# Performance work log

Hardware: AMD Instinct MI355X
Metric: run time of the kernel (lower is better)

## Reference

```python
import jax, jax.numpy as jnp
import numpy as np
from jax import lax

B_, L_, D_ = 4, 2048, 256
DI, NS, DC, DTR = 512, 16, 4, 16  # d_inner=2*D, d_state, d_conv, dt_rank=ceil(D/16)
DFF = 4 * D_


def setup_inputs():
    key = jax.random.key(0)
    ks = jax.random.split(key, 20)
    rn = lambda k, s, sc=0.02: jax.random.normal(k, s, jnp.float32) * sc
    return {
        "x": jax.random.normal(ks[0], (B_, L_, D_), jnp.float32),
        "in_proj_w": rn(ks[1], (2 * DI, D_)), "in_proj_b": jnp.zeros((2 * DI,), jnp.float32),
        "conv_w": rn(ks[2], (DI, DC), 0.1), "conv_b": jnp.zeros((DI,), jnp.float32),
        "x_proj_w": rn(ks[3], (DTR + 2 * NS, DI)),
        "dt_proj_w": rn(ks[4], (DI, DTR), 0.1), "dt_proj_b": rn(ks[5], (DI,), 0.5),
        "A_log": jnp.log(jnp.tile(jnp.arange(1, NS + 1, dtype=jnp.float32), (DI, 1))),
        "D_ssm": jnp.ones((DI,), jnp.float32),
        "out_proj_w": rn(ks[6], (D_, DI)), "out_proj_b": jnp.zeros((D_,), jnp.float32),
        "ln1_g": jnp.ones((D_,), jnp.float32), "ln1_b": jnp.zeros((D_,), jnp.float32),
        "fc1_w": rn(ks[7], (DFF, D_)), "fc1_b": jnp.zeros((DFF,), jnp.float32),
        "fc2_w": rn(ks[8], (D_, DFF)), "fc2_b": jnp.zeros((D_,), jnp.float32),
        "ln2_g": jnp.ones((D_,), jnp.float32), "ln2_b": jnp.zeros((D_,), jnp.float32),
    }


def _layer_norm(x, g, b, eps=1e-5):
    m = jnp.mean(x, -1, keepdims=True)
    v = jnp.mean((x - m) ** 2, -1, keepdims=True)
    return (x - m) / jnp.sqrt(v + eps) * g + b


def _mamba(x, in_proj_w, in_proj_b, conv_w, conv_b, x_proj_w, dt_proj_w, dt_proj_b, A_log, D_ssm, out_proj_w, out_proj_b):
    B, L, D = x.shape
    xz = x @ in_proj_w.T + in_proj_b                       # [B,L,2*DI]
    xi, z = jnp.split(xz, 2, axis=-1)
    # causal depthwise conv over time
    xc = jnp.transpose(xi, (0, 2, 1))                       # [B,DI,L]
    xc = lax.conv_general_dilated(xc, conv_w[:, None, :], (1,), [(DC - 1, 0)],
                                  dimension_numbers=("NCH", "OIH", "NCH"),
                                  feature_group_count=DI)
    xi = jax.nn.silu(jnp.transpose(xc + conv_b[None, :, None], (0, 2, 1)))  # [B,L,DI]
    x_dbl = xi @ x_proj_w.T                                 # [B,L,DTR+2*NS]
    dt, Bs, Cs = jnp.split(x_dbl, [DTR, DTR + NS], axis=-1)
    dt = jax.nn.softplus(dt @ dt_proj_w.T + dt_proj_b)      # [B,L,DI]
    A = -jnp.exp(A_log)                                     # [DI,NS]
    dA = jnp.exp(dt[..., None] * A)                         # [B,L,DI,NS]
    dBu = dt[..., None] * Bs[:, :, None, :] * xi[..., None]  # [B,L,DI,NS]
    dA_t = jnp.moveaxis(dA, 1, 0)
    dBu_t = jnp.moveaxis(dBu, 1, 0)
    C_t = jnp.moveaxis(Cs, 1, 0)                            # [L,B,NS]

    def step(h, inp):
        a, bu, c = inp
        h = a * h + bu                                      # [B,DI,NS]
        y = jnp.einsum("bdn,bn->bd", h, c)
        return h, y

    h0 = jnp.zeros((B, DI, NS), x.dtype)
    _, ys = lax.scan(step, h0, (dA_t, dBu_t, C_t))
    y = jnp.moveaxis(ys, 0, 1) + xi * D_ssm                 # [B,L,DI]
    y = y * jax.nn.silu(z)
    return y @ out_proj_w.T + out_proj_b


def reference(x, in_proj_w, in_proj_b, conv_w, conv_b, x_proj_w, dt_proj_w, dt_proj_b,
              A_log, D_ssm, out_proj_w, out_proj_b, ln1_g, ln1_b, fc1_w, fc1_b,
              fc2_w, fc2_b, ln2_g, ln2_b):
    gelu = lambda t: jax.nn.gelu(t, approximate=False)
    ssm = _mamba(x, in_proj_w, in_proj_b, conv_w, conv_b, x_proj_w, dt_proj_w,
                 dt_proj_b, A_log, D_ssm, out_proj_w, out_proj_b)
    y = _layer_norm(x + ssm, ln1_g, ln1_b)                  # dropout = identity (eval)
    ffn = gelu(gelu(y @ fc1_w.T + fc1_b) @ fc2_w.T + fc2_b)
    return _layer_norm(y + ffn, ln2_g, ln2_b)
```

## Files before the change

kernel.cpp:

```cpp
#include <hip/hip_runtime.h>

typedef __bf16 bf16x8 __attribute__((ext_vector_type(8)));
typedef float  f32x4  __attribute__((ext_vector_type(4)));

#define AS1 __attribute__((address_space(1)))
#define AS3 __attribute__((address_space(3)))

__device__ __forceinline__ float bf2f(ushort u) {
    union { unsigned int i; float f; } v; v.i = ((unsigned int)u) << 16; return v.f;
}
__device__ __forceinline__ ushort f2bf(float f) {
    union { float f; unsigned int i; } v; v.f = f;
    unsigned int i = v.i;
    unsigned int r = i + 0x7FFFu + ((i >> 16) & 1u);
    return (ushort)(r >> 16);
}
__device__ __forceinline__ float bflo(unsigned int u) { return bf2f((ushort)(u & 0xFFFFu)); }
__device__ __forceinline__ float bfhi(unsigned int u) { return bf2f((ushort)(u >> 16)); }
__device__ __forceinline__ float gelu_f(float v) {
    return 0.5f * v * (1.f + erff(v * 0.70710678118654752f));
}

__device__ __forceinline__ bool sniff_inline(const ushort* __restrict__ x) {
    const int lane = threadIdx.x & 63;
    int cnt = 0;
    #pragma unroll
    for (int r = 0; r < 4; r++) {
        const ushort u = x[lane + r * 64];
        const int e = (u >> 7) & 0xFF;
        if ((u & 0x7FFF) == 0 || (e >= 112 && e <= 141)) cnt++;
    }
    #pragma unroll
    for (int o = 32; o > 0; o >>= 1) cnt += __shfl_xor(cnt, o);
    return cnt >= 224;
}

struct CanonArgs {
    const void* src[20];
    int off[20];
    int total;
};

__launch_bounds__(256)
__global__ void canon_k(CanonArgs a, ushort* __restrict__ dst, ushort* __restrict__ xpw_pad,
                        const ushort* __restrict__ sniffx)
{
    const int i = blockIdx.x * 256 + threadIdx.x;
    if (i >= a.total) {
        const int j = i - a.total;
        if (j < 8192) xpw_pad[24576 + j] = 0;
        return;
    }
    const bool fl = sniff_inline(sniffx);
    int s = 0;
    #pragma unroll
    for (int t = 1; t < 20; t++) if (i >= a.off[t]) s = t;
    const int li = i - a.off[s];
    ushort v;
    if (fl) v = ((const ushort*)a.src[s])[li];
    else    v = f2bf(((const float*)a.src[s])[li]);
    dst[i] = v;
    if (s == 5) xpw_pad[li] = v;
}

template<int BM, int BN>
__launch_bounds__(256, 2)
__global__ void gemm_bt(const ushort* __restrict__ A, const ushort* __restrict__ W,
                        const ushort* __restrict__ bias, ushort* __restrict__ Cb,
                        int N, int K)
{
    constexpr int WMT = BM / 32;
    constexpr int WNT = BN / 32;
    __shared__ __align__(16) ushort As[BM * 32];
    __shared__ __align__(16) ushort Bs[BN * 32];
    const int tid  = threadIdx.x;
    const int wave = tid >> 6;
    const int lane = tid & 63;
    const int m0 = blockIdx.x * BM;
    const int n0 = blockIdx.y * BN;
    const int wm = (wave >> 1) * (BM / 2);
    const int wn = (wave & 1) * (BN / 2);
    const int lrow = lane & 15;
    const int quad = lane >> 4;

    f32x4 acc[WMT][WNT];
    #pragma unroll
    for (int i = 0; i < WMT; i++)
        #pragma unroll
        for (int j = 0; j < WNT; j++)
            #pragma unroll
            for (int r = 0; r < 4; r++) acc[i][j][r] = 0.f;

    for (int k0 = 0; k0 < K; k0 += 32) {
        #pragma unroll
        for (int t = 0; t < BM / 64; t++) {
            const int inst = t * 4 + wave;
            const int row  = inst * 16 + (lane >> 2);
            const int sub  = lane & 3;
            const ushort* gp = A + (size_t)(m0 + row) * K + (k0 + sub * 8);
            __builtin_amdgcn_global_load_lds((AS1 void*)(void*)gp,
                                             (AS3 void*)(As + inst * 512), 16, 0, 0);
        }
        #pragma unroll
        for (int t = 0; t < BN / 64; t++) {
            const int inst = t * 4 + wave;
            const int row  = inst * 16 + (lane >> 2);
            const int sub  = lane & 3;
            const ushort* gp = W + (size_t)(n0 + row) * K + (k0 + sub * 8);
            __builtin_amdgcn_global_load_lds((AS1 void*)(void*)gp,
                                             (AS3 void*)(Bs + inst * 512), 16, 0, 0);
        }
        __syncthreads();
        bf16x8 afr[WMT], bfr[WNT];
        #pragma unroll
        for (int i = 0; i < WMT; i++)
            afr[i] = *(const bf16x8*)&As[(wm + i * 16 + lrow) * 32 + quad * 8];
        #pragma unroll
        for (int j = 0; j < WNT; j++)
            bfr[j] = *(const bf16x8*)&Bs[(wn + j * 16 + lrow) * 32 + quad * 8];
        #pragma unroll
        for (int i = 0; i < WMT; i++)
            #pragma unroll
            for (int j = 0; j < WNT; j++)
                acc[i][j] = __builtin_amdgcn_mfma_f32_16x16x32_bf16(afr[i], bfr[j], acc[i][j], 0, 0, 0);
        __syncthreads();
    }

    #pragma unroll
    for (int i = 0; i < WMT; i++) {
        const int gm = m0 + wm + i * 16 + quad * 4;
        #pragma unroll
        for (int j = 0; j < WNT; j++) {
            const int gn = n0 + wn + j * 16 + lrow;
            const float bv = bf2f(bias[gn]);
            #pragma unroll
            for (int r = 0; r < 4; r++)
                Cb[(size_t)(gm + r) * N + gn] = f2bf(acc[i][j][r] + bv);
        }
    }
}

__launch_bounds__(512)
__global__ void convscan1_k(const ushort* __restrict__ xz, const ushort* __restrict__ cw,
                            const ushort* __restrict__ cb, const ushort* __restrict__ xpw_pad,
                            const ushort* __restrict__ dtw, const ushort* __restrict__ dtb,
                            const ushort* __restrict__ Alog,
                            float* __restrict__ xdbl, float* __restrict__ summh,
                            float* __restrict__ sdt32, float* __restrict__ hhalf,
                            float* __restrict__ sdthalf)
{
    __shared__ __align__(16) ushort xcs[32 * 520];
    __shared__ float XD[32 * 48];
    const int tid  = threadIdx.x;
    const int wave = tid >> 6;
    const int lane = tid & 63;
    const int lrow = lane & 15;
    const int quad = lane >> 4;
    const int c = blockIdx.x, b = blockIdx.y;
    const int t0 = b * 2048 + c * 32;

    {
        const int d8 = (tid & 63) * 8;
        ushort wl[32];
        *(uint4*)&wl[0]  = *(const uint4*)&cw[d8 * 4];
        *(uint4*)&wl[8]  = *(const uint4*)&cw[d8 * 4 + 8];
        *(uint4*)&wl[16] = *(const uint4*)&cw[d8 * 4 + 16];
        *(uint4*)&wl[24] = *(const uint4*)&cw[d8 * 4 + 24];
        ushort bl[8];
        *(uint4*)&bl[0] = *(const uint4*)&cb[d8];
        #pragma unroll
        for (int it = 0; it < 4; it++) {
            const int trow = it * 8 + wave;
            const int t = t0 + trow;
            const int l = t & 2047;
            float acc[8];
            #pragma unroll
            for (int j = 0; j < 8; j++) acc[j] = bf2f(bl[j]);
            #pragma unroll
            for (int k = 0; k < 4; k++) {
                const int ls = l - 3 + k;
                if (ls >= 0) {
                    ushort xl[8];
                    *(uint4*)&xl[0] = *(const uint4*)&xz[(size_t)(t - 3 + k) * 1024 + d8];
                    #pragma unroll
                    for (int j = 0; j < 8; j++) acc[j] += bf2f(xl[j]) * bf2f(wl[j * 4 + k]);
                }
            }
            ushort ol[8];
            #pragma unroll
            for (int j = 0; j < 8; j++) {
                const float s = acc[j] / (1.f + __expf(-acc[j]));
                ol[j] = f2bf(s);
            }
            *(uint4*)&xcs[trow * 520 + d8] = *(uint4*)&ol[0];
        }
    }
    __syncthreads();

    {
        const int mt = wave >> 2, nt = wave & 3;
        const ushort* bptr = xpw_pad + (size_t)(nt * 16 + lrow) * 512 + quad * 8;
        f32x4 acc = {0.f, 0.f, 0.f, 0.f};
        #pragma unroll
        for (int hh = 0; hh < 2; hh++) {
            bf16x8 Bv[8];
            #pragma unroll
            for (int s = 0; s < 8; s++)
                Bv[s] = *(const bf16x8*)(bptr + hh * 256 + s * 32);
            #pragma unroll
            for (int s = 0; s < 8; s++) {
                const bf16x8 afr = *(const bf16x8*)&xcs[(mt * 16 + lrow) * 520 + hh * 256 + s * 32 + quad * 8];
                acc = __builtin_amdgcn_mfma_f32_16x16x32_bf16(afr, Bv[s], acc, 0, 0, 0);
            }
        }
        const int col = nt * 16 + lrow;
        if (col < 48) {
            #pragma unroll
            for (int r = 0; r < 4; r++) {
                const int row = mt * 16 + quad * 4 + r;
                XD[row * 48 + col] = acc[r];
                xdbl[(size_t)(t0 + row) * 64 + col] = acc[r];
            }
        }
    }
    __syncthreads();

    {
        const int d = tid;
        const uint4 w0 = *(const uint4*)&dtw[d * 16];
        const uint4 w1 = *(const uint4*)&dtw[d * 16 + 8];
        const float wd[16] = { bflo(w0.x), bfhi(w0.x), bflo(w0.y), bfhi(w0.y),
                               bflo(w0.z), bfhi(w0.z), bflo(w0.w), bfhi(w0.w),
                               bflo(w1.x), bfhi(w1.x), bflo(w1.y), bfhi(w1.y),
                               bflo(w1.z), bfhi(w1.z), bflo(w1.w), bfhi(w1.w) };
        const float dtbv = bf2f(dtb[d]);
        float A[16], h[16];
        #pragma unroll
        for (int n = 0; n < 16; n++) {
            A[n] = -__expf(bf2f(Alog[d * 16 + n]));
            h[n] = 0.f;
        }
        const size_t bh = ((size_t)(b * 64 + c) * 16) * 512 + d;
        const size_t bs = (size_t)(b * 64 + c) * 512 + d;
        float sdt = 0.f;
        for (int i = 0; i < 32; i++) {
            const float* Xr = &XD[i * 48];
            float s0 = dtbv, s1 = 0.f, s2 = 0.f, s3 = 0.f;
            #pragma unroll
            for (int k = 0; k < 16; k += 4) {
                s0 += Xr[k]     * wd[k];
                s1 += Xr[k + 1] * wd[k + 1];
                s2 += Xr[k + 2] * wd[k + 2];
                s3 += Xr[k + 3] * wd[k + 3];
            }
            const float s = (s0 + s1) + (s2 + s3);
            const float dtv = (s > 15.f) ? s : __logf(1.f + __expf(s));
            const float xiv = bf2f(xcs[i * 520 + d]);
            const float dx = dtv * xiv;
            sdt += dtv;
            #pragma unroll
            for (int n = 0; n < 16; n++) {
                const float da = __expf(dtv * A[n]);
                h[n] = da * h[n] + dx * Xr[16 + n];
            }
            if (i == 15) {
                #pragma unroll
                for (int n = 0; n < 16; n++) hhalf[bh + (size_t)n * 512] = h[n];
                sdthalf[bs] = sdt;
            }
        }
        #pragma unroll
        for (int n = 0; n < 16; n++) summh[bh + (size_t)n * 512] = h[n];
        sdt32[bs] = sdt;
    }
}

__launch_bounds__(128)
__global__ void combine_k(float* __restrict__ summh, const float* __restrict__ sdt32,
                          const ushort* __restrict__ Alog)
{
    const int b  = blockIdx.x >> 6;
    const int n  = (blockIdx.x >> 2) & 15;
    const int dq = blockIdx.x & 3;
    const int d  = dq * 128 + threadIdx.x;
    const float An = -__expf(bf2f(Alog[d * 16 + n]));
    float h = 0.f;
    #pragma unroll
    for (int q = 0; q < 2; q++) {
        float p[32], hl[32], ho[32];
        #pragma unroll
        for (int c2 = 0; c2 < 32; c2++) {
            const int cc = q * 32 + c2;
            hl[c2] = summh[((size_t)(b * 64 + cc) * 16 + n) * 512 + d];
            p[c2]  = __expf(An * sdt32[(size_t)(b * 64 + cc) * 512 + d]);
        }
        #pragma unroll
        for (int c2 = 0; c2 < 32; c2++) {
            ho[c2] = h;
            h = p[c2] * h + hl[c2];
        }
        #pragma unroll
        for (int c2 = 0; c2 < 32; c2++)
            summh[((size_t)(b * 64 + (q * 32 + c2)) * 16 + n) * 512 + d] = ho[c2];
    }
}

__launch_bounds__(512, 4)
__global__ void tail_k(const ushort* __restrict__ xz, const ushort* __restrict__ cw,
                       const ushort* __restrict__ cb, const float* __restrict__ xdbl,
                       const ushort* __restrict__ dtw, const ushort* __restrict__ dtb,
                       const ushort* __restrict__ Alog, const float* __restrict__ summh,
                       const float* __restrict__ hhalf, const float* __restrict__ sdthalf,
                       const ushort* __restrict__ Dssm, const ushort* __restrict__ cx,
                       const ushort* __restrict__ opw, const ushort* __restrict__ opb,
                       const ushort* __restrict__ ln1g, const ushort* __restrict__ ln1b,
                       const ushort* __restrict__ f1w, const ushort* __restrict__ f1b,
                       const ushort* __restrict__ f2w, const ushort* __restrict__ f2b,
                       const ushort* __restrict__ ln2g, const ushort* __restrict__ ln2b,
                       void* __restrict__ dout, const ushort* __restrict__ sniffx)
{
    __shared__ __align__(16) ushort yls[16 * 520];
    __shared__ float XD[16 * 48];
    __shared__ __align__(16) ushort y1bs[16 * 264];
    __shared__ float redS[8 * 16], redQ[8 * 16];
    ushort* f1q = yls;

    const int tid  = threadIdx.x;
    const int wave = tid >> 6;
    const int lane = tid & 63;
    const int lrow = lane & 15;
    const int quad = lane >> 4;
    const int c = blockIdx.x, b = blockIdx.y;
    const int t0 = b * 2048 + c * 16;
    const int n0w = wave * 32;

    {
        const int d8 = (tid & 63) * 8;
        ushort wl[32];
        *(uint4*)&wl[0]  = *(const uint4*)&cw[d8 * 4];
        *(uint4*)&wl[8]  = *(const uint4*)&cw[d8 * 4 + 8];
        *(uint4*)&wl[16] = *(const uint4*)&cw[d8 * 4 + 16];
        *(uint4*)&wl[24] = *(const uint4*)&cw[d8 * 4 + 24];
        ushort bl[8];
        *(uint4*)&bl[0] = *(const uint4*)&cb[d8];
        #pragma unroll
        for (int it = 0; it < 2; it++) {
            const int trow = it * 8 + wave;
            const int t = t0 + trow;
            const int l = t & 2047;
            float acc[8];
            #pragma unroll
            for (int j = 0; j < 8; j++) acc[j] = bf2f(bl[j]);
            #pragma unroll
            for (int k = 0; k < 4; k++) {
                const int ls = l - 3 + k;
                if (ls >= 0) {
                    ushort xl[8];
                    *(uint4*)&xl[0] = *(const uint4*)&xz[(size_t)(t - 3 + k) * 1024 + d8];
                    #pragma unroll
                    for (int j = 0; j < 8; j++) acc[j] += bf2f(xl[j]) * bf2f(wl[j * 4 + k]);
                }
            }
            ushort ol[8];
            #pragma unroll
            for (int j = 0; j < 8; j++) {
                const float s = acc[j] / (1.f + __expf(-acc[j]));
                ol[j] = f2bf(s);
            }
            *(uint4*)&yls[trow * 520 + d8] = *(uint4*)&ol[0];
        }
    }
    for (int e = tid; e < 768; e += 512)
        XD[e] = xdbl[(size_t)(t0 + (e / 48)) * 64 + (e % 48)];
    __syncthreads();

    {
        const int d = tid;
        const uint4 w0 = *(const uint4*)&dtw[d * 16];
        const uint4 w1 = *(const uint4*)&dtw[d * 16 + 8];
        const float wd[16] = { bflo(w0.x), bfhi(w0.x), bflo(w0.y), bfhi(w0.y),
                               bflo(w0.z), bfhi(w0.z), bflo(w0.w), bfhi(w0.w),
                               bflo(w1.x), bfhi(w1.x), bflo(w1.y), bfhi(w1.y),
                               bflo(w1.z), bfhi(w1.z), bflo(w1.w), bfhi(w1.w) };
        const float dtbv = bf2f(dtb[d]);
        float A[16], h[16];
        #pragma unroll
        for (int n = 0; n < 16; n++) A[n] = -__expf(bf2f(Alog[d * 16 + n]));
        const int c32 = c >> 1;
        const size_t bh = ((size_t)(b * 64 + c32) * 16) * 512 + d;
        #pragma unroll
        for (int n = 0; n < 16; n++) h[n] = summh[bh + (size_t)n * 512];
        if (c & 1) {
            const float sdth = sdthalf[(size_t)(b * 64 + c32) * 512 + d];
            #pragma unroll
            for (int n = 0; n < 16; n++)
                h[n] = __expf(A[n] * sdth) * h[n] + hhalf[bh + (size_t)n * 512];
        }
        const float Dv = bf2f(Dssm[d]);
        for (int i = 0; i < 16; i++) {
            const int t = t0 + i;
            const float* Xr = &XD[i * 48];
            float s0 = dtbv, s1 = 0.f, s2 = 0.f, s3 = 0.f;
            #pragma unroll
            for (int k = 0; k < 16; k += 4) {
                s0 += Xr[k]     * wd[k];
                s1 += Xr[k + 1] * wd[k + 1];
                s2 += Xr[k + 2] * wd[k + 2];
                s3 += Xr[k + 3] * wd[k + 3];
            }
            const float s = (s0 + s1) + (s2 + s3);
            const float dtv = (s > 15.f) ? s : __logf(1.f + __expf(s));
            const float xiv = bf2f(yls[i * 520 + d]);
            const float dx = dtv * xiv;
            float yv0 = 0.f, yv1 = 0.f;
            #pragma unroll
            for (int n = 0; n < 16; n += 2) {
                const float da0 = __expf(dtv * A[n]);
                const float da1 = __expf(dtv * A[n + 1]);
                h[n]     = da0 * h[n]     + dx * Xr[16 + n];
                h[n + 1] = da1 * h[n + 1] + dx * Xr[17 + n];
                yv0 += h[n]     * Xr[32 + n];
                yv1 += h[n + 1] * Xr[33 + n];
            }
            float yv = yv0 + yv1;
            yv += xiv * Dv;
            const float zv = bf2f(xz[(size_t)t * 1024 + 512 + d]);
            yv *= zv / (1.f + __expf(-zv));
            yls[i * 520 + d] = f2bf(yv);
        }
    }
    __syncthreads();

    f32x4 accP[2];
    #pragma unroll
    for (int j = 0; j < 2; j++)
        #pragma unroll
        for (int r = 0; r < 4; r++) accP[j][r] = 0.f;
    {
        const ushort* bp0 = opw + (size_t)(n0w + lrow) * 512 + quad * 8;
        const ushort* bp1 = opw + (size_t)(n0w + 16 + lrow) * 512 + quad * 8;
        #pragma unroll
        for (int hh = 0; hh < 2; hh++) {
            bf16x8 B0[8], B1[8];
            #pragma unroll
            for (int s = 0; s < 8; s++) {
                B0[s] = *(const bf16x8*)(bp0 + hh * 256 + s * 32);
                B1[s] = *(const bf16x8*)(bp1 + hh * 256 + s * 32);
            }
            #pragma unroll
            for (int s = 0; s < 8; s++) {
                const bf16x8 afr = *(const bf16x8*)&yls[lrow * 520 + hh * 256 + s * 32 + quad * 8];
                accP[0] = __builtin_amdgcn_mfma_f32_16x16x32_bf16(afr, B0[s], accP[0], 0, 0, 0);
                accP[1] = __builtin_amdgcn_mfma_f32_16x16x32_bf16(afr, B1[s], accP[1], 0, 0, 0);
            }
        }
    }
    float vP[2][4];
    float ps[4], pq[4];
    #pragma unroll
    for (int r = 0; r < 4; r++) { ps[r] = 0.f; pq[r] = 0.f; }
    #pragma unroll
    for (int j = 0; j < 2; j++) {
        const int col = n0w + j * 16 + lrow;
        const float bv = bf2f(opb[col]);
        #pragma unroll
        for (int r = 0; r < 4; r++) {
            const int row = quad * 4 + r;
            float v = accP[j][r] + bv + bf2f(cx[(size_t)(t0 + row) * 256 + col]);
            vP[j][r] = v;
            ps[r] += v;
            pq[r] += v * v;
        }
    }
    #pragma unroll
    for (int r = 0; r < 4; r++) {
        #pragma unroll
        for (int o = 8; o > 0; o >>= 1) {
            ps[r] += __shfl_xor(ps[r], o);
            pq[r] += __shfl_xor(pq[r], o);
        }
        if (lrow == 0) {
            const int row = quad * 4 + r;
            redS[wave * 16 + row] = ps[r];
            redQ[wave * 16 + row] = pq[r];
        }
    }
    __syncthreads();

    float y1f[2][4];
    #pragma unroll
    for (int r = 0; r < 4; r++) {
        const int row = quad * 4 + r;
        float S = 0.f, Q = 0.f;
        #pragma unroll
        for (int w = 0; w < 8; w++) { S += redS[w * 16 + row]; Q += redQ[w * 16 + row]; }
        const float mean = S * (1.f / 256.f);
        const float var  = Q * (1.f / 256.f) - mean * mean;
        const float rs   = rsqrtf(var + 1e-5f);
        #pragma unroll
        for (int j = 0; j < 2; j++) {
            const int col = n0w + j * 16 + lrow;
            const float o2 = (vP[j][r] - mean) * rs * bf2f(ln1g[col]) + bf2f(ln1b[col]);
            y1f[j][r] = o2;
            y1bs[row * 264 + col] = f2bf(o2);
        }
    }
    __syncthreads();

    f32x4 acc2[2];
    #pragma unroll
    for (int j = 0; j < 2; j++)
        #pragma unroll
        for (int r = 0; r < 4; r++) acc2[j][r] = 0.f;

    for (int q = 0; q < 4; q++) {
        f32x4 a1[2];
        #pragma unroll
        for (int j = 0; j < 2; j++)
            #pragma unroll
            for (int r = 0; r < 4; r++) a1[j][r] = 0.f;
        {
            const ushort* bp0 = f1w + (size_t)(q * 256 + n0w + lrow) * 256 + quad * 8;
            const ushort* bp1 = f1w + (size_t)(q * 256 + n0w + 16 + lrow) * 256 + quad * 8;
            bf16x8 B0[8], B1[8];
            #pragma unroll
            for (int s = 0; s < 8; s++) {
                B0[s] = *(const bf16x8*)(bp0 + s * 32);
                B1[s] = *(const bf16x8*)(bp1 + s * 32);
            }
            #pragma unroll
            for (int s = 0; s < 8; s++) {
                const bf16x8 afr = *(const bf16x8*)&y1bs[lrow * 264 + s * 32 + quad * 8];
                a1[0] = __builtin_amdgcn_mfma_f32_16x16x32_bf16(afr, B0[s], a1[0], 0, 0, 0);
                a1[1] = __builtin_amdgcn_mfma_f32_16x16x32_bf16(afr, B1[s], a1[1], 0, 0, 0);
            }
        }
        #pragma unroll
        for (int j = 0; j < 2; j++) {
            const int qc = n0w + j * 16 + lrow;
            const float bv = bf2f(f1b[q * 256 + qc]);
            #pragma unroll
            for (int r = 0; r < 4; r++) {
                const int row = quad * 4 + r;
                f1q[row * 260 + qc] = f2bf(gelu_f(a1[j][r] + bv));
            }
        }
        __syncthreads();
        {
            const ushort* bp0 = f2w + (size_t)(n0w + lrow) * 1024 + q * 256 + quad * 8;
            const ushort* bp1 = f2w + (size_t)(n0w + 16 + lrow) * 1024 + q * 256 + quad * 8;
            bf16x8 B0[8], B1[8];
            #pragma unroll
            for (int s = 0; s < 8; s++) {
                B0[s] = *(const bf16x8*)(bp0 + s * 32);
                B1[s] = *(const bf16x8*)(bp1 + s * 32);
            }
            #pragma unroll
            for (int s = 0; s < 8; s++) {
                const bf16x8 afr = *(const bf16x8*)&f1q[lrow * 260 + s * 32 + quad * 8];
                acc2[0] = __builtin_amdgcn_mfma_f32_16x16x32_bf16(afr, B0[s], acc2[0], 0, 0, 0);
                acc2[1] = __builtin_amdgcn_mfma_f32_16x16x32_bf16(afr, B1[s], acc2[1], 0, 0, 0);
            }
        }
        __syncthreads();
    }

    float v2[2][4];
    #pragma unroll
    for (int r = 0; r < 4; r++) { ps[r] = 0.f; pq[r] = 0.f; }
    #pragma unroll
    for (int j = 0; j < 2; j++) {
        const int col = n0w + j * 16 + lrow;
        const float bv = bf2f(f2b[col]);
        #pragma unroll
        for (int r = 0; r < 4; r++) {
            const float v = gelu_f(acc2[j][r] + bv) + y1f[j][r];
            v2[j][r] = v;
            ps[r] += v;
            pq[r] += v * v;
        }
    }
    #pragma unroll
    for (int r = 0; r < 4; r++) {
        #pragma unroll
        for (int o = 8; o > 0; o >>= 1) {
            ps[r] += __shfl_xor(ps[r], o);
            pq[r] += __shfl_xor(pq[r], o);
        }
        if (lrow == 0) {
            const int row = quad * 4 + r;
            redS[wave * 16 + row] = ps[r];
            redQ[wave * 16 + row] = pq[r];
        }
    }
    __syncthreads();

    const bool fl = sniff_inline(sniffx);
    #pragma unroll
    for (int r = 0; r < 4; r++) {
        const int row = quad * 4 + r;
        float S = 0.f, Q = 0.f;
        #pragma unroll
        for (int w = 0; w < 8; w++) { S += redS[w * 16 + row]; Q += redQ[w * 16 + row]; }
        const float mean = S * (1.f / 256.f);
        const float var  = Q * (1.f / 256.f) - mean * mean;
        const float rs   = rsqrtf(var + 1e-5f);
        #pragma unroll
        for (int j = 0; j < 2; j++) {
            const int col = n0w + j * 16 + lrow;
            const size_t off = (size_t)(t0 + row) * 256 + col;
            const float o2 = (v2[j][r] - mean) * rs * bf2f(ln2g[col]) + bf2f(ln2b[col]);
            if (fl) ((ushort*)dout)[off] = f2bf(o2);
            else    ((float*)dout)[off]  = o2;
        }
    }
}

extern "C" void kernel_launch(void* const* d_in, const int* in_sizes, int n_in,
                              void* d_out, int out_size, void* d_ws, size_t ws_size,
                              hipStream_t stream)
{
    char* ws = (char*)d_ws;
    ushort* canon = (ushort*)(ws + 256);

    static const int coff[20] = {
        0,        2097152,  2359296,  2360320,  2362368,
        2362880,  2387456,  2395648,  2396160,  2404352,
        2404864,  2535936,  2536192,  2536448,  2536704,
        2798848,  2799872,  3062016,  3062272,  3062528 };
    static const int ctot = 3062784;

    CanonArgs ca;
    for (int i = 0; i < 20; i++) { ca.src[i] = d_in[i]; ca.off[i] = coff[i]; }
    ca.total = ctot;

    const ushort* cx   = canon + coff[0];
    const ushort* cipw = canon + coff[1];
    const ushort* cipb = canon + coff[2];
    const ushort* ccw  = canon + coff[3];
    const ushort* ccb  = canon + coff[4];
    const ushort* cdtw = canon + coff[6];
    const ushort* cdtb = canon + coff[7];
    const ushort* calog= canon + coff[8];
    const ushort* cdssm= canon + coff[9];
    const ushort* copw = canon + coff[10];
    const ushort* copb = canon + coff[11];
    const ushort* cln1g= canon + coff[12];
    const ushort* cln1b= canon + coff[13];
    const ushort* cf1w = canon + coff[14];
    const ushort* cf1b = canon + coff[15];
    const ushort* cf2w = canon + coff[16];
    const ushort* cf2b = canon + coff[17];
    const ushort* cln2g= canon + coff[18];
    const ushort* cln2b= canon + coff[19];

    ushort* xpw_pad = (ushort*)(ws + 6291456);
    ushort* xz      = (ushort*)(ws + 8388608);
    float*  xdbl    = (float*)(ws + 25165824);
    float*  summh   = (float*)(ws + 27262976);
    float*  hhalf   = (float*)(ws + 35651584);
    float*  sdt32   = (float*)(ws + 44040192);
    float*  sdthalf = (float*)(ws + 44564480);
    const ushort* sx = (const ushort*)d_in[0];

    canon_k<<<(ctot + 8192 + 255) / 256, 256, 0, stream>>>(ca, canon, xpw_pad, sx);
    gemm_bt<128, 128><<<dim3(64, 8), 256, 0, stream>>>(cx, cipw, cipb, xz, 1024, 256);
    convscan1_k<<<dim3(64, 4), 512, 0, stream>>>(
        xz, ccw, ccb, xpw_pad, cdtw, cdtb, calog, xdbl, summh, sdt32, hhalf, sdthalf);
    combine_k<<<256, 128, 0, stream>>>(summh, sdt32, calog);
    tail_k<<<dim3(128, 4), 512, 0, stream>>>(
        xz, ccw, ccb, xdbl, cdtw, cdtb, calog, summh, hhalf, sdthalf, cdssm, cx,
        copw, copb, cln1g, cln1b, cf1w, cf1b, cf2w, cf2b, cln2g, cln2b,
        d_out, sx);
}
```

Baseline: 255.5 us.

## Split conv/scan pipeline into separate kernels with finer 16-step chunks

Replaces the fused conv+scan1 kernel and the tail kernel's scan prologue with separate conv/x_proj, scan1, combine and scan2 kernels. Chunks shrink from 32 to 16 timesteps and the channel dimension is split across blocks, so the serial scans run on more, smaller blocks (1024 instead of 256). The conv output is materialised to global memory and scan2 writes gated y back into xz, which the FFN kernel then reads. This adds two kernel launches and extra global traffic but removes the duplicated conv work and the half-chunk fixup in the tail kernel, and shortens the per-block serial dependency chain.

```diff
diff --git a/kernel.cpp b/kernel.cpp
--- a/kernel.cpp
+++ b/kernel.cpp
@@ -141,23 +141,18 @@
 }
 
 __launch_bounds__(512)
-__global__ void convscan1_k(const ushort* __restrict__ xz, const ushort* __restrict__ cw,
-                            const ushort* __restrict__ cb, const ushort* __restrict__ xpw_pad,
-                            const ushort* __restrict__ dtw, const ushort* __restrict__ dtb,
-                            const ushort* __restrict__ Alog,
-                            float* __restrict__ xdbl, float* __restrict__ summh,
-                            float* __restrict__ sdt32, float* __restrict__ hhalf,
-                            float* __restrict__ sdthalf)
-{
-    __shared__ __align__(16) ushort xcs[32 * 520];
-    __shared__ float XD[32 * 48];
+__global__ void convx_k(const ushort* __restrict__ xz, const ushort* __restrict__ cw,
+                        const ushort* __restrict__ cb, const ushort* __restrict__ xpw_pad,
+                        ushort* __restrict__ xc, float* __restrict__ xdbl)
+{
+    __shared__ __align__(16) ushort xcs[16 * 520];
     const int tid  = threadIdx.x;
     const int wave = tid >> 6;
     const int lane = tid & 63;
     const int lrow = lane & 15;
     const int quad = lane >> 4;
     const int c = blockIdx.x, b = blockIdx.y;
-    const int t0 = b * 2048 + c * 32;
+    const int t0 = b * 2048 + c * 16;
 
     {
         const int d8 = (tid & 63) * 8;
@@ -169,7 +164,7 @@
         ushort bl[8];
         *(uint4*)&bl[0] = *(const uint4*)&cb[d8];
         #pragma unroll
-        for (int it = 0; it < 4; it++) {
+        for (int it = 0; it < 2; it++) {
             const int trow = it * 8 + wave;
             const int t = t0 + trow;
             const int l = t & 2047;
@@ -197,8 +192,8 @@
     }
     __syncthreads();
 
-    {
-        const int mt = wave >> 2, nt = wave & 3;
+    if (wave < 3) {
+        const int nt = wave;
         const ushort* bptr = xpw_pad + (size_t)(nt * 16 + lrow) * 512 + quad * 8;
         f32x4 acc = {0.f, 0.f, 0.f, 0.f};
         #pragma unroll
@@ -209,74 +204,88 @@
                 Bv[s] = *(const bf16x8*)(bptr + hh * 256 + s * 32);
             #pragma unroll
             for (int s = 0; s < 8; s++) {
-                const bf16x8 afr = *(const bf16x8*)&xcs[(mt * 16 + lrow) * 520 + hh * 256 + s * 32 + quad * 8];
+                const bf16x8 afr = *(const bf16x8*)&xcs[lrow * 520 + hh * 256 + s * 32 + quad * 8];
                 acc = __builtin_amdgcn_mfma_f32_16x16x32_bf16(afr, Bv[s], acc, 0, 0, 0);
             }
         }
         const int col = nt * 16 + lrow;
         if (col < 48) {
             #pragma unroll
-            for (int r = 0; r < 4; r++) {
-                const int row = mt * 16 + quad * 4 + r;
-                XD[row * 48 + col] = acc[r];
-                xdbl[(size_t)(t0 + row) * 64 + col] = acc[r];
-            }
-        }
-    }
+            for (int r = 0; r < 4; r++)
+                xdbl[(size_t)(t0 + quad * 4 + r) * 64 + col] = acc[r];
+        }
+    }
+
+    {
+        const int row = tid >> 5;
+        const int col = (tid & 31) * 16;
+        *(uint4*)&xc[(size_t)(t0 + row) * 512 + col]     = *(const uint4*)&xcs[row * 520 + col];
+        *(uint4*)&xc[(size_t)(t0 + row) * 512 + col + 8] = *(const uint4*)&xcs[row * 520 + col + 8];
+    }
+}
+
+__launch_bounds__(256)
+__global__ void scan1_k(const ushort* __restrict__ xc, const float* __restrict__ xdbl,
+                        const ushort* __restrict__ dtw, const ushort* __restrict__ dtb,
+                        const ushort* __restrict__ Alog,
+                        float* __restrict__ summh, float* __restrict__ sdtb)
+{
+    __shared__ float XD[16 * 48];
+    const int tid = threadIdx.x;
+    const int c = blockIdx.x, dh = blockIdx.y, b = blockIdx.z;
+    const int t0 = b * 2048 + c * 16;
+    const int d = dh * 256 + tid;
+
+    for (int e = tid; e < 768; e += 256)
+        XD[e] = xdbl[(size_t)(t0 + (e / 48)) * 64 + (e % 48)];
     __syncthreads();
 
-    {
-        const int d = tid;
-        const uint4 w0 = *(const uint4*)&dtw[d * 16];
-        const uint4 w1 = *(const uint4*)&dtw[d * 16 + 8];
-        const float wd[16] = { bflo(w0.x), bfhi(w0.x), bflo(w0.y), bfhi(w0.y),
-                               bflo(w0.z), bfhi(w0.z), bflo(w0.w), bfhi(w0.w),
-                               bflo(w1.x), bfhi(w1.x), bflo(w1.y), bfhi(w1.y),
-                               bflo(w1.z), bfhi(w1.z), bflo(w1.w), bfhi(w1.w) };
-        const float dtbv = bf2f(dtb[d]);
-        float A[16], h[16];
+    const uint4 w0 = *(const uint4*)&dtw[d * 16];
+    const uint4 w1 = *(const uint4*)&dtw[d * 16 + 8];
+    const float wd[16] = { bflo(w0.x), bfhi(w0.x), bflo(w0.y), bfhi(w0.y),
+                           bflo(w0.z), bfhi(w0.z), bflo(w0.w), bfhi(w0.w),
+                           bflo(w1.x), bfhi(w1.x), bflo(w1.y), bfhi(w1.y),
+                           bflo(w1.z), bfhi(w1.z), bflo(w1.w), bfhi(w1.w) };
+    const uint4 a0 = *(const uint4*)&Alog[d * 16];
+    const uint4 a1 = *(const uint4*)&Alog[d * 16 + 8];
+    const float al[16] = { bflo(a0.x), bfhi(a0.x), bflo(a0.y), bfhi(a0.y),
+                           bflo(a0.z), bfhi(a0.z), bflo(a0.w), bfhi(a0.w),
+                           bflo(a1.x), bfhi(a1.x), bflo(a1.y), bfhi(a1.y),
+                           bflo(a1.z), bfhi(a1.z), bflo(a1.w), bfhi(a1.w) };
+    const float dtbv = bf2f(dtb[d]);
+    float A[16], h[16];
+    #pragma unroll
+    for (int n = 0; n < 16; n++) { A[n] = -__expf(al[n]); h[n] = 0.f; }
+    float sdt = 0.f;
+    for (int i = 0; i < 16; i++) {
+        const float* Xr = &XD[i * 48];
+        float s0 = dtbv, s1 = 0.f, s2 = 0.f, s3 = 0.f;
+        #pragma unroll
+        for (int k = 0; k < 16; k += 4) {
+            s0 += Xr[k]     * wd[k];
+            s1 += Xr[k + 1] * wd[k + 1];
+            s2 += Xr[k + 2] * wd[k + 2];
+            s3 += Xr[k + 3] * wd[k + 3];
+        }
+        const float s = (s0 + s1) + (s2 + s3);
+        const float dtv = (s > 15.f) ? s : __logf(1.f + __expf(s));
+        const float xiv = bf2f(xc[(size_t)(t0 + i) * 512 + d]);
+        const float dx = dtv * xiv;
+        sdt += dtv;
         #pragma unroll
         for (int n = 0; n < 16; n++) {
-            A[n] = -__expf(bf2f(Alog[d * 16 + n]));
-            h[n] = 0.f;
-        }
-        const size_t bh = ((size_t)(b * 64 + c) * 16) * 512 + d;
-        const size_t bs = (size_t)(b * 64 + c) * 512 + d;
-        float sdt = 0.f;
-        for (int i = 0; i < 32; i++) {
-            const float* Xr = &XD[i * 48];
-            float s0 = dtbv, s1 = 0.f, s2 = 0.f, s3 = 0.f;
-            #pragma unroll
-            for (int k = 0; k < 16; k += 4) {
-                s0 += Xr[k]     * wd[k];
-                s1 += Xr[k + 1] * wd[k + 1];
-                s2 += Xr[k + 2] * wd[k + 2];
-                s3 += Xr[k + 3] * wd[k + 3];
-            }
-            const float s = (s0 + s1) + (s2 + s3);
-            const float dtv = (s > 15.f) ? s : __logf(1.f + __expf(s));
-            const float xiv = bf2f(xcs[i * 520 + d]);
-            const float dx = dtv * xiv;
-            sdt += dtv;
-            #pragma unroll
-            for (int n = 0; n < 16; n++) {
-                const float da = __expf(dtv * A[n]);
-                h[n] = da * h[n] + dx * Xr[16 + n];
-            }
-            if (i == 15) {
-                #pragma unroll
-                for (int n = 0; n < 16; n++) hhalf[bh + (size_t)n * 512] = h[n];
-                sdthalf[bs] = sdt;
-            }
-        }
-        #pragma unroll
-        for (int n = 0; n < 16; n++) summh[bh + (size_t)n * 512] = h[n];
-        sdt32[bs] = sdt;
-    }
+            const float da = __expf(dtv * A[n]);
+            h[n] = da * h[n] + dx * Xr[16 + n];
+        }
+    }
+    const size_t bh = ((size_t)(b * 128 + c) * 16) * 512 + d;
+    #pragma unroll
+    for (int n = 0; n < 16; n++) summh[bh + (size_t)n * 512] = h[n];
+    sdtb[(size_t)(b * 128 + c) * 512 + d] = sdt;
 }
 
 __launch_bounds__(128)
-__global__ void combine_k(float* __restrict__ summh, const float* __restrict__ sdt32,
+__global__ void combine_k(float* __restrict__ summh, const float* __restrict__ sdtb,
                           const ushort* __restrict__ Alog)
 {
     const int b  = blockIdx.x >> 6;
@@ -286,13 +295,13 @@
     const float An = -__expf(bf2f(Alog[d * 16 + n]));
     float h = 0.f;
     #pragma unroll
-    for (int q = 0; q < 2; q++) {
+    for (int q = 0; q < 4; q++) {
         float p[32], hl[32], ho[32];
         #pragma unroll
         for (int c2 = 0; c2 < 32; c2++) {
             const int cc = q * 32 + c2;
-            hl[c2] = summh[((size_t)(b * 64 + cc) * 16 + n) * 512 + d];
-            p[c2]  = __expf(An * sdt32[(size_t)(b * 64 + cc) * 512 + d]);
+            hl[c2] = summh[((size_t)(b * 128 + cc) * 16 + n) * 512 + d];
+            p[c2]  = __expf(An * sdtb[(size_t)(b * 128 + cc) * 512 + d]);
         }
         #pragma unroll
         for (int c2 = 0; c2 < 32; c2++) {
@@ -301,26 +310,91 @@
         }
         #pragma unroll
         for (int c2 = 0; c2 < 32; c2++)
-            summh[((size_t)(b * 64 + (q * 32 + c2)) * 16 + n) * 512 + d] = ho[c2];
+            summh[((size_t)(b * 128 + (q * 32 + c2)) * 16 + n) * 512 + d] = ho[c2];
+    }
+}
+
+__launch_bounds__(256)
+__global__ void scan2_k(ushort* __restrict__ xz, const ushort* __restrict__ xc,
+                        const float* __restrict__ xdbl,
+                        const ushort* __restrict__ dtw, const ushort* __restrict__ dtb,
+                        const ushort* __restrict__ Alog, const float* __restrict__ summh,
+                        const ushort* __restrict__ Dssm)
+{
+    __shared__ float XD[16 * 48];
+    const int tid = threadIdx.x;
+    const int c = blockIdx.x, dh = blockIdx.y, b = blockIdx.z;
+    const int t0 = b * 2048 + c * 16;
+    const int d = dh * 256 + tid;
+
+    for (int e = tid; e < 768; e += 256)
+        XD[e] = xdbl[(size_t)(t0 + (e / 48)) * 64 + (e % 48)];
+    __syncthreads();
+
+    const uint4 w0 = *(const uint4*)&dtw[d * 16];
+    const uint4 w1 = *(const uint4*)&dtw[d * 16 + 8];
+    const float wd[16] = { bflo(w0.x), bfhi(w0.x), bflo(w0.y), bfhi(w0.y),
+                           bflo(w0.z), bfhi(w0.z), bflo(w0.w), bfhi(w0.w),
+                           bflo(w1.x), bfhi(w1.x), bflo(w1.y), bfhi(w1.y),
+                           bflo(w1.z), bfhi(w1.z), bflo(w1.w), bfhi(w1.w) };
+    const uint4 a0 = *(const uint4*)&Alog[d * 16];
+    const uint4 a1 = *(const uint4*)&Alog[d * 16 + 8];
+    const float al[16] = { bflo(a0.x), bfhi(a0.x), bflo(a0.y), bfhi(a0.y),
+                           bflo(a0.z), bfhi(a0.z), bflo(a0.w), bfhi(a0.w),
+                           bflo(a1.x), bfhi(a1.x), bflo(a1.y), bfhi(a1.y),
+                           bflo(a1.z), bfhi(a1.z), bflo(a1.w), bfhi(a1.w) };
+    const float dtbv = bf2f(dtb[d]);
+    float A[16], h[16];
+    #pragma unroll
+    for (int n = 0; n < 16; n++) A[n] = -__expf(al[n]);
+    const size_t bh = ((size_t)(b * 128 + c) * 16) * 512 + d;
+    #pragma unroll
+    for (int n = 0; n < 16; n++) h[n] = summh[bh + (size_t)n * 512];
+    const float Dv = bf2f(Dssm[d]);
+
+    for (int i = 0; i < 16; i++) {
+        const int t = t0 + i;
+        const float* Xr = &XD[i * 48];
+        float s0 = dtbv, s1 = 0.f, s2 = 0.f, s3 = 0.f;
+        #pragma unroll
+        for (int k = 0; k < 16; k += 4) {
+            s0 += Xr[k]     * wd[k];
+            s1 += Xr[k + 1] * wd[k + 1];
+            s2 += Xr[k + 2] * wd[k + 2];
+            s3 += Xr[k + 3] * wd[k + 3];
+        }
+        const float s = (s0 + s1) + (s2 + s3);
+        const float dtv = (s > 15.f) ? s : __logf(1.f + __expf(s));
+        const float xiv = bf2f(xc[(size_t)t * 512 + d]);
+        const float dx = dtv * xiv;
+        float yv0 = 0.f, yv1 = 0.f;
+        #pragma unroll
+        for (int n = 0; n < 16; n += 2) {
+            const float da0 = __expf(dtv * A[n]);
+            const float da1 = __expf(dtv * A[n + 1]);
+            h[n]     = da0 * h[n]     + dx * Xr[16 + n];
+            h[n + 1] = da1 * h[n + 1] + dx * Xr[17 + n];
+            yv0 += h[n]     * Xr[32 + n];
+            yv1 += h[n + 1] * Xr[33 + n];
+        }
+        float yv = yv0 + yv1;
+        yv += xiv * Dv;
+        const float zv = bf2f(xz[(size_t)t * 1024 + 512 + d]);
+        yv *= zv / (1.f + __expf(-zv));
+        xz[(size_t)t * 1024 + d] = f2bf(yv);
     }
 }
 
 __launch_bounds__(512, 4)
-__global__ void tail_k(const ushort* __restrict__ xz, const ushort* __restrict__ cw,
-                       const ushort* __restrict__ cb, const float* __restrict__ xdbl,
-                       const ushort* __restrict__ dtw, const ushort* __restrict__ dtb,
-                       const ushort* __restrict__ Alog, const float* __restrict__ summh,
-                       const float* __restrict__ hhalf, const float* __restrict__ sdthalf,
-                       const ushort* __restrict__ Dssm, const ushort* __restrict__ cx,
-                       const ushort* __restrict__ opw, const ushort* __restrict__ opb,
-                       const ushort* __restrict__ ln1g, const ushort* __restrict__ ln1b,
-                       const ushort* __restrict__ f1w, const ushort* __restrict__ f1b,
-                       const ushort* __restrict__ f2w, const ushort* __restrict__ f2b,
-                       const ushort* __restrict__ ln2g, const ushort* __restrict__ ln2b,
-                       void* __restrict__ dout, const ushort* __restrict__ sniffx)
+__global__ void ffn_k(const ushort* __restrict__ xz, const ushort* __restrict__ cx,
+                      const ushort* __restrict__ opw, const ushort* __restrict__ opb,
+                      const ushort* __restrict__ ln1g, const ushort* __restrict__ ln1b,
+                      const ushort* __restrict__ f1w, const ushort* __restrict__ f1b,
+                      const ushort* __restrict__ f2w, const ushort* __restrict__ f2b,
+                      const ushort* __restrict__ ln2g, const ushort* __restrict__ ln2b,
+                      void* __restrict__ dout, const ushort* __restrict__ sniffx)
 {
     __shared__ __align__(16) ushort yls[16 * 520];
-    __shared__ float XD[16 * 48];
     __shared__ __align__(16) ushort y1bs[16 * 264];
     __shared__ float redS[8 * 16], redQ[8 * 16];
     ushort* f1q = yls;
@@ -335,99 +409,10 @@
     const int n0w = wave * 32;
 
     {
-        const int d8 = (tid & 63) * 8;
-        ushort wl[32];
-        *(uint4*)&wl[0]  = *(const uint4*)&cw[d8 * 4];
-        *(uint4*)&wl[8]  = *(const uint4*)&cw[d8 * 4 + 8];
-        *(uint4*)&wl[16] = *(const uint4*)&cw[d8 * 4 + 16];
-        *(uint4*)&wl[24] = *(const uint4*)&cw[d8 * 4 + 24];
-        ushort bl[8];
-        *(uint4*)&bl[0] = *(const uint4*)&cb[d8];
-        #pragma unroll
-        for (int it = 0; it < 2; it++) {
-            const int trow = it * 8 + wave;
-            const int t = t0 + trow;
-            const int l = t & 2047;
-            float acc[8];
-            #pragma unroll
-            for (int j = 0; j < 8; j++) acc[j] = bf2f(bl[j]);
-            #pragma unroll
-            for (int k = 0; k < 4; k++) {
-                const int ls = l - 3 + k;
-                if (ls >= 0) {
-                    ushort xl[8];
-                    *(uint4*)&xl[0] = *(const uint4*)&xz[(size_t)(t - 3 + k) * 1024 + d8];
-                    #pragma unroll
-                    for (int j = 0; j < 8; j++) acc[j] += bf2f(xl[j]) * bf2f(wl[j * 4 + k]);
-                }
-            }
-            ushort ol[8];
-            #pragma unroll
-            for (int j = 0; j < 8; j++) {
-                const float s = acc[j] / (1.f + __expf(-acc[j]));
-                ol[j] = f2bf(s);
-            }
-            *(uint4*)&yls[trow * 520 + d8] = *(uint4*)&ol[0];
-        }
-    }
-    for (int e = tid; e < 768; e += 512)
-        XD[e] = xdbl[(size_t)(t0 + (e / 48)) * 64 + (e % 48)];
-    __syncthreads();
-
-    {
-        const int d = tid;
-        const uint4 w0 = *(const uint4*)&dtw[d * 16];
-        const uint4 w1 = *(const uint4*)&dtw[d * 16 + 8];
-        const float wd[16] = { bflo(w0.x), bfhi(w0.x), bflo(w0.y), bfhi(w0.y),
-                               bflo(w0.z), bfhi(w0.z), bflo(w0.w), bfhi(w0.w),
-                               bflo(w1.x), bfhi(w1.x), bflo(w1.y), bfhi(w1.y),
-                               bflo(w1.z), bfhi(w1.z), bflo(w1.w), bfhi(w1.w) };
-        const float dtbv = bf2f(dtb[d]);
-        float A[16], h[16];
-        #pragma unroll
-        for (int n = 0; n < 16; n++) A[n] = -__expf(bf2f(Alog[d * 16 + n]));
-        const int c32 = c >> 1;
-        const size_t bh = ((size_t)(b * 64 + c32) * 16) * 512 + d;
-        #pragma unroll
-        for (int n = 0; n < 16; n++) h[n] = summh[bh + (size_t)n * 512];
-        if (c & 1) {
-            const float sdth = sdthalf[(size_t)(b * 64 + c32) * 512 + d];
-            #pragma unroll
-            for (int n = 0; n < 16; n++)
-                h[n] = __expf(A[n] * sdth) * h[n] + hhalf[bh + (size_t)n * 512];
-        }
-        const float Dv = bf2f(Dssm[d]);
-        for (int i = 0; i < 16; i++) {
-            const int t = t0 + i;
-            const float* Xr = &XD[i * 48];
-            float s0 = dtbv, s1 = 0.f, s2 = 0.f, s3 = 0.f;
-            #pragma unroll
-            for (int k = 0; k < 16; k += 4) {
-                s0 += Xr[k]     * wd[k];
-                s1 += Xr[k + 1] * wd[k + 1];
-                s2 += Xr[k + 2] * wd[k + 2];
-                s3 += Xr[k + 3] * wd[k + 3];
-            }
-            const float s = (s0 + s1) + (s2 + s3);
-            const float dtv = (s > 15.f) ? s : __logf(1.f + __expf(s));
-            const float xiv = bf2f(yls[i * 520 + d]);
-            const float dx = dtv * xiv;
-            float yv0 = 0.f, yv1 = 0.f;
-            #pragma unroll
-            for (int n = 0; n < 16; n += 2) {
-                const float da0 = __expf(dtv * A[n]);
-                const float da1 = __expf(dtv * A[n + 1]);
-                h[n]     = da0 * h[n]     + dx * Xr[16 + n];
-                h[n + 1] = da1 * h[n + 1] + dx * Xr[17 + n];
-                yv0 += h[n]     * Xr[32 + n];
-                yv1 += h[n + 1] * Xr[33 + n];
-            }
-            float yv = yv0 + yv1;
-            yv += xiv * Dv;
-            const float zv = bf2f(xz[(size_t)t * 1024 + 512 + d]);
-            yv *= zv / (1.f + __expf(-zv));
-            yls[i * 520 + d] = f2bf(yv);
-        }
+        const int row = tid >> 5;
+        const int col = (tid & 31) * 16;
+        *(uint4*)&yls[row * 520 + col]     = *(const uint4*)&xz[(size_t)(t0 + row) * 1024 + col];
+        *(uint4*)&yls[row * 520 + col + 8] = *(const uint4*)&xz[(size_t)(t0 + row) * 1024 + col + 8];
     }
     __syncthreads();
 
@@ -658,18 +643,17 @@
     ushort* xz      = (ushort*)(ws + 8388608);
     float*  xdbl    = (float*)(ws + 25165824);
     float*  summh   = (float*)(ws + 27262976);
-    float*  hhalf   = (float*)(ws + 35651584);
-    float*  sdt32   = (float*)(ws + 44040192);
-    float*  sdthalf = (float*)(ws + 44564480);
+    float*  sdtb    = (float*)(ws + 44040192);
+    ushort* xc      = (ushort*)(ws + 45088768);
     const ushort* sx = (const ushort*)d_in[0];
 
     canon_k<<<(ctot + 8192 + 255) / 256, 256, 0, stream>>>(ca, canon, xpw_pad, sx);
     gemm_bt<128, 128><<<dim3(64, 8), 256, 0, stream>>>(cx, cipw, cipb, xz, 1024, 256);
-    convscan1_k<<<dim3(64, 4), 512, 0, stream>>>(
-        xz, ccw, ccb, xpw_pad, cdtw, cdtb, calog, xdbl, summh, sdt32, hhalf, sdthalf);
-    combine_k<<<256, 128, 0, stream>>>(summh, sdt32, calog);
-    tail_k<<<dim3(128, 4), 512, 0, stream>>>(
-        xz, ccw, ccb, xdbl, cdtw, cdtb, calog, summh, hhalf, sdthalf, cdssm, cx,
-        copw, copb, cln1g, cln1b, cf1w, cf1b, cf2w, cf2b, cln2g, cln2b,
+    convx_k<<<dim3(128, 4), 512, 0, stream>>>(xz, ccw, ccb, xpw_pad, xc, xdbl);
+    scan1_k<<<dim3(128, 2, 4), 256, 0, stream>>>(xc, xdbl, cdtw, cdtb, calog, summh, sdtb);
+    combine_k<<<256, 128, 0, stream>>>(summh, sdtb, calog);
+    scan2_k<<<dim3(128, 2, 4), 256, 0, stream>>>(xz, xc, xdbl, cdtw, cdtb, calog, summh, cdssm);
+    ffn_k<<<dim3(128, 4), 512, 0, stream>>>(
+        xz, cx, copw, copb, cln1g, cln1b, cf1w, cf1b, cf2w, cf2b, cln2g, cln2b,
         d_out, sx);
 }
```

After: 274.0 us. +7.3%, slower.
